# Optimization experiments

Measured on AMD Instinct MI355X. Metric: run time of the kernel, lower is better.

The kernel has to match this reference:

```python
import jax, jax.numpy as jnp
import numpy as np

N = 50000
E = 800000
D_IN = 64
D_HID = 64
N_CLASS = 40


def setup_inputs() -> dict:
    key = jax.random.key(0)
    ks = jax.random.split(key, 9)
    x = jax.random.normal(ks[0], (N, D_IN), dtype=jnp.float32)
    edge_index = jax.random.randint(ks[1], (2, E), 0, N, dtype=jnp.int64)
    # GCNConv weights (glorot-ish scale) and biases
    W1 = jax.random.normal(ks[2], (D_IN, D_HID), dtype=jnp.float32) / np.sqrt(D_IN)
    b1 = jnp.zeros((D_HID,), dtype=jnp.float32)
    W2 = jax.random.normal(ks[3], (D_HID, D_HID), dtype=jnp.float32) / np.sqrt(D_HID)
    b2 = jnp.zeros((D_HID,), dtype=jnp.float32)
    Wc = jax.random.normal(ks[4], (D_HID, N_CLASS), dtype=jnp.float32) / np.sqrt(D_HID)
    bc = jnp.zeros((N_CLASS,), dtype=jnp.float32)
    return {"x": x, "edge_index": edge_index, "W1": W1, "b1": b1,
            "W2": W2, "b2": b2, "Wc": Wc, "bc": bc}


def _gcn_conv(x, W, b, src, dst, n_nodes):
    """PyG GCNConv: add self-loops, sym-normalized mean aggregation, then +bias.
    out = D^{-1/2} (A + I) D^{-1/2} X W + b
    src/dst already include self-loops."""
    h = x @ W  # [N, D_out] -- transform before aggregation (fewer FLOPs if D_out<=D_in)
    deg = jax.ops.segment_sum(jnp.ones_like(dst, dtype=h.dtype), dst, num_segments=n_nodes)
    dinv = jnp.where(deg > 0, jax.lax.rsqrt(deg), 0.0)  # [N]
    norm = dinv[src] * dinv[dst]  # [E+N]
    msg = h[src] * norm[:, None]  # gather + scale
    out = jax.ops.segment_sum(msg, dst, num_segments=n_nodes)  # scatter-add
    return out + b


def reference(x, edge_index, W1, b1, W2, b2, Wc, bc):
    n = x.shape[0]
    loops = jnp.arange(n, dtype=edge_index.dtype)
    src = jnp.concatenate([edge_index[0], loops])
    dst = jnp.concatenate([edge_index[1], loops])
    h = jnp.tanh(_gcn_conv(x, W1, b1, src, dst, n))
    h = jnp.tanh(_gcn_conv(h, W2, b2, src, dst, n))
    out = h @ Wc + bc
    return (out, h)
```

## Files before the change

### kernel.cpp

```cpp
#include <hip/hip_runtime.h>
#include <math.h>

#define NN 50000
#define NE 800000
#define D 64
#define NC 40
#define NBUCK 196
#define SLAB 16384
#define EPB 4096

typedef unsigned short u16;
typedef unsigned int u32;

__device__ __forceinline__ u16 f32_to_bf16(float v) {
    u32 x = __float_as_uint(v);
    x += 0x7FFFu + ((x >> 16) & 1u);
    return (u16)(x >> 16);
}
__device__ __forceinline__ float bflo(u32 v) { return __uint_as_float(v << 16); }
__device__ __forceinline__ float bfhi(u32 v) { return __uint_as_float(v & 0xffff0000u); }


__global__ __launch_bounds__(256) void bucket_scatter(const int* __restrict__ ei,
                                                      int* __restrict__ cursor,
                                                      u32* __restrict__ slab) {
    __shared__ int sums[256];
    __shared__ int lofs[256];
    __shared__ int lcur[256];
    __shared__ int gbase[256];
    __shared__ int tot_s;
    __shared__ u32 sorted[EPB];
    __shared__ int gdest[EPB];
    int tid = threadIdx.x;

    u32 pk[16];
    int nmine = 0;
    int e0 = blockIdx.x * EPB + tid * 16;
    if (e0 < NE) {
        nmine = 16;
#pragma unroll
        for (int j = 0; j < 4; ++j) {
            int4 ss = *(const int4*)&ei[e0 + j * 4];
            int4 dd = *(const int4*)&ei[NE + e0 + j * 4];
            pk[j * 4 + 0] = ((u32)dd.x << 16) | (u32)ss.x;
            pk[j * 4 + 1] = ((u32)dd.y << 16) | (u32)ss.y;
            pk[j * 4 + 2] = ((u32)dd.z << 16) | (u32)ss.z;
            pk[j * 4 + 3] = ((u32)dd.w << 16) | (u32)ss.w;
        }
    }

    sums[tid] = 0;
    __syncthreads();
    for (int j = 0; j < nmine; ++j) atomicAdd(&sums[pk[j] >> 24], 1);
    __syncthreads();
    int v = sums[tid];
    __syncthreads();
    for (int off = 1; off < 256; off <<= 1) {
        int u = (tid >= off) ? sums[tid - off] : 0;
        __syncthreads();
        sums[tid] += u;
        __syncthreads();
    }
    lofs[tid] = sums[tid] - v;
    lcur[tid] = sums[tid] - v;
    if (tid == 255) tot_s = sums[255];
    if (tid < NBUCK) gbase[tid] = atomicAdd(&cursor[tid], v);
    __syncthreads();

    for (int j = 0; j < nmine; ++j) {
        u32 p = pk[j];
        int bin = (int)(p >> 24);
        int pos = atomicAdd(&lcur[bin], 1);
        sorted[pos] = p;
        gdest[pos] = bin * SLAB + gbase[bin] + (pos - lofs[bin]);
    }
    __syncthreads();

    int tot = tot_s;
    for (int i = tid; i < tot; i += 256) slab[gdest[i]] = sorted[i];
}


__global__ __launch_bounds__(256) void ell_build(const u32* __restrict__ slab,
                                                 const int* __restrict__ cursor,
                                                 u16* __restrict__ ell,
                                                 int* __restrict__ cnt,
                                                 float* __restrict__ dinv) {
    __shared__ u16 ell_lds[256 * 64];
    __shared__ int cnt_lds[256];
    int b = blockIdx.x, tid = threadIdx.x;
    uint4* z = (uint4*)ell_lds;
    for (int i = tid; i < 2048; i += 256) z[i] = make_uint4(0, 0, 0, 0);
    cnt_lds[tid] = 0;
    __syncthreads();

    int nE = cursor[b];
    const u32* run = slab + b * SLAB;
    int base = b * 256;
    for (int i = tid; i < nE; i += 256) {
        u32 p = run[i];
        int dl = (int)(p >> 16) - base;
        int r = atomicAdd(&cnt_lds[dl], 1);
        if (r < 64) ell_lds[dl * 64 + r] = (u16)(p & 0xffffu);
    }
    __syncthreads();

    int nNodes = NN - base; if (nNodes > 256) nNodes = 256;
    const uint4* s4 = (const uint4*)ell_lds;
    uint4* d4 = (uint4*)(ell + (size_t)base * 64);
    int n4 = nNodes * 8;
    for (int i = tid; i < n4; i += 256) d4[i] = s4[i];
    if (tid < nNodes) {
        int c = cnt_lds[tid];
        cnt[base + tid] = c;
        dinv[base + tid] = rsqrtf((float)c + 1.0f);
    }
}


__global__ __launch_bounds__(256) void gemm64_bf16(const float* __restrict__ A,
                                                   const float* __restrict__ W,
                                                   const float* __restrict__ dinv,
                                                   u16* __restrict__ C) {
    __shared__ float Ws[64 * 64];
    __shared__ float As[4 * 64];
    int tid = threadIdx.x;
    for (int i = tid; i < 64 * 64; i += 256) Ws[i] = W[i];
    int r = tid >> 6, c = tid & 63;
    int row = blockIdx.x * 4 + r;
    if (row < NN) As[r * 64 + c] = A[row * 64 + c];
    __syncthreads();
    if (row < NN) {
        float acc = 0.0f;
#pragma unroll
        for (int k = 0; k < 64; ++k) acc += As[r * 64 + k] * Ws[k * 64 + c];
        C[row * 64 + c] = f32_to_bf16(acc * dinv[row]);
    }
}


__device__ __forceinline__ void gather_pair_ell(const u16* __restrict__ ell,
                                                const int* __restrict__ cnt,
                                                const u32* __restrict__ hs32,
                                                int n0, int half, int p,
                                                u32* __restrict__ idxh,
                                                float& ox, float& oy) {
    int node = n0 + half;
    int deg0 = cnt[n0];     if (deg0 > 64) deg0 = 64;
    int deg1 = cnt[n0 + 1]; if (deg1 > 64) deg1 = 64;
    int deg = half ? deg1 : deg0;
    int degmax = (deg0 > deg1) ? deg0 : deg1;
    const u16* row = ell + node * 64;

    u32 sv = hs32[node * 32 + p];
    float ax = bflo(sv), ay = bfhi(sv);
    float bx = 0.0f, by = 0.0f;

    for (int base = 0; base < degmax; base += 32) {
        int slot = base + p;
        idxh[p] = (slot < deg) ? (u32)row[slot] : (u32)node;
        __builtin_amdgcn_wave_barrier();
        int n = degmax - base;
        if (n > 32) n = 32;
        for (int m0 = 0; m0 < n; m0 += 8) {
            u32 st[8];
#pragma unroll
            for (int u = 0; u < 8; ++u) {
                int src = (int)idxh[m0 + u];
                st[u] = hs32[src * 32 + p];
            }
#pragma unroll
            for (int u = 0; u < 8; ++u) {
                bool act = (base + m0 + u) < deg;
                float vx = act ? bflo(st[u]) : 0.0f;
                float vy = act ? bfhi(st[u]) : 0.0f;
                if (u & 1) { bx += vx; by += vy; } else { ax += vx; ay += vy; }
            }
        }
        __builtin_amdgcn_wave_barrier();
    }
    ox = ax + bx;
    oy = ay + by;
}


__global__ __launch_bounds__(256) void gather_l1_fused(const u16* __restrict__ ell,
                                                       const int* __restrict__ cnt,
                                                       const u16* __restrict__ hs,
                                                       const float* __restrict__ dinv,
                                                       const float* __restrict__ b1,
                                                       const float* __restrict__ W2,
                                                       u16* __restrict__ hs_out) {
    __shared__ float Ws[64 * 64];
    __shared__ __align__(16) float hb[4][2][64];
    __shared__ u32 idxb[4][2][32];
    int tid = threadIdx.x;
    for (int i = tid; i < 64 * 64; i += 256) Ws[i] = W2[i];
    __syncthreads();

    int r = tid >> 6, l = tid & 63, half = l >> 5, p = l & 31;
    int n0 = (blockIdx.x * 4 + r) * 2;
    int node = n0 + half;

    float gx, gy;
    gather_pair_ell(ell, cnt, (const u32*)hs, n0, half, p, idxb[r][half], gx, gy);

    float dv = dinv[node];
    float2 bb = *(const float2*)&b1[2 * p];
    float hx = tanhf(gx * dv + bb.x);
    float hy = tanhf(gy * dv + bb.y);
    *(float2*)&hb[r][half][2 * p] = make_float2(hx, hy);
    __builtin_amdgcn_wave_barrier();

    int d = l;
    float dv0 = dinv[n0], dv1 = dinv[n0 + 1];
    float acc0 = 0.0f, acc1 = 0.0f;
#pragma unroll
    for (int k4 = 0; k4 < 16; ++k4) {
        float4 h0 = *(const float4*)&hb[r][0][k4 * 4];
        float4 h1 = *(const float4*)&hb[r][1][k4 * 4];
        float w0 = Ws[(k4 * 4 + 0) * 64 + d];
        float w1 = Ws[(k4 * 4 + 1) * 64 + d];
        float w2 = Ws[(k4 * 4 + 2) * 64 + d];
        float w3 = Ws[(k4 * 4 + 3) * 64 + d];
        acc0 += h0.x * w0 + h0.y * w1 + h0.z * w2 + h0.w * w3;
        acc1 += h1.x * w0 + h1.y * w1 + h1.z * w2 + h1.w * w3;
    }
    hs_out[n0 * 64 + d] = f32_to_bf16(acc0 * dv0);
    hs_out[(n0 + 1) * 64 + d] = f32_to_bf16(acc1 * dv1);
}

__global__ __launch_bounds__(256) void gather_l2_fused(const u16* __restrict__ ell,
                                                       const int* __restrict__ cnt,
                                                       const u16* __restrict__ hs,
                                                       const float* __restrict__ dinv,
                                                       const float* __restrict__ b2,
                                                       const float* __restrict__ Wc,
                                                       const float* __restrict__ bc,
                                                       float* __restrict__ h_out,
                                                       float* __restrict__ out) {
    __shared__ float Ws[64 * NC];
    __shared__ float bs[NC];
    __shared__ __align__(16) float hb[4][2][64];
    __shared__ u32 idxb[4][2][32];
    int tid = threadIdx.x;
    for (int i = tid; i < 64 * NC; i += 256) Ws[i] = Wc[i];
    if (tid < NC) bs[tid] = bc[tid];
    __syncthreads();

    int r = tid >> 6, l = tid & 63, half = l >> 5, p = l & 31;
    int n0 = (blockIdx.x * 4 + r) * 2;
    int node = n0 + half;

    float gx, gy;
    gather_pair_ell(ell, cnt, (const u32*)hs, n0, half, p, idxb[r][half], gx, gy);

    float dv = dinv[node];
    float2 bb = *(const float2*)&b2[2 * p];
    float hx = tanhf(gx * dv + bb.x);
    float hy = tanhf(gy * dv + bb.y);
    *(float2*)&h_out[node * 64 + 2 * p] = make_float2(hx, hy);
    *(float2*)&hb[r][half][2 * p] = make_float2(hx, hy);
    __builtin_amdgcn_wave_barrier();

    int d = l;
    int dc = (d < NC) ? d : NC - 1;
    float acc0 = bs[dc], acc1 = bs[dc];
#pragma unroll
    for (int k4 = 0; k4 < 16; ++k4) {
        float4 v0 = *(const float4*)&hb[r][0][k4 * 4];
        float4 v1 = *(const float4*)&hb[r][1][k4 * 4];
        float w0 = Ws[(k4 * 4 + 0) * NC + dc];
        float w1 = Ws[(k4 * 4 + 1) * NC + dc];
        float w2 = Ws[(k4 * 4 + 2) * NC + dc];
        float w3 = Ws[(k4 * 4 + 3) * NC + dc];
        acc0 += v0.x * w0 + v0.y * w1 + v0.z * w2 + v0.w * w3;
        acc1 += v1.x * w0 + v1.y * w1 + v1.z * w2 + v1.w * w3;
    }
    if (d < NC) {
        out[n0 * NC + d] = acc0;
        out[(n0 + 1) * NC + d] = acc1;
    }
}


extern "C" void kernel_launch(void* const* d_in, const int* in_sizes, int n_in,
                              void* d_out, int out_size, void* d_ws, size_t ws_size,
                              hipStream_t stream) {
    const float* x  = (const float*)d_in[0];
    const int*   ei = (const int*)d_in[1];
    const float* W1 = (const float*)d_in[2];
    const float* b1 = (const float*)d_in[3];
    const float* W2 = (const float*)d_in[4];
    const float* b2 = (const float*)d_in[5];
    const float* Wc = (const float*)d_in[6];
    const float* bc = (const float*)d_in[7];

    float* out   = (float*)d_out;
    float* h_out = out + NN * NC;

    u32*   slab   = (u32*)d_ws;
    int*   cursor = (int*)(slab + NBUCK * SLAB);
    int*   cnt    = cursor + 256;
    float* dinv   = (float*)(cnt + NN);
    u16*   ell    = (u16*)(dinv + NN);
    u16*   hsA    = ell + (size_t)NN * 64;
    u16*   hsB    = hsA + NN * D;

    const int scatBlocks  = (NE + EPB - 1) / EPB;
    const int nodeBlocks4 = (NN + 3) / 4;
    const int nodeBlocks8 = NN / 8;

    hipMemsetAsync(cursor, 0, NBUCK * sizeof(int), stream);
    bucket_scatter<<<scatBlocks, 256, 0, stream>>>(ei, cursor, slab);
    ell_build<<<NBUCK, 256, 0, stream>>>(slab, cursor, ell, cnt, dinv);

    gemm64_bf16<<<nodeBlocks4, 256, 0, stream>>>(x, W1, dinv, hsA);
    gather_l1_fused<<<nodeBlocks8, 256, 0, stream>>>(ell, cnt, hsA, dinv, b1, W2, hsB);
    gather_l2_fused<<<nodeBlocks8, 256, 0, stream>>>(ell, cnt, hsB, dinv, b2, Wc, bc,
                                                     h_out, out);
}
```

Before: 186.8 us.

## Gather four nodes per wave with 8-byte loads and shuffle-broadcast indices

The ELL gather is restructured so each 64-lane wave handles four nodes, 16 lanes per node, each lane loading 4 bf16 features (uint2) per neighbor. The LDS index staging and wave barriers are replaced by one vector load of the ELL row per lane plus __shfl broadcasts of packed 16-bit indices, with 16 outstanding loads per iteration. The fused dense epilogues now compute four output rows per wave, reusing each weight load across more nodes. Waves now run to the maximum degree of four nodes instead of two, which adds more masked work per wave.

```diff
diff --git a/kernel.cpp b/kernel.cpp
--- a/kernel.cpp
+++ b/kernel.cpp
@@ -139,48 +139,48 @@
 }
 
 
-__device__ __forceinline__ void gather_pair_ell(const u16* __restrict__ ell,
-                                                const int* __restrict__ cnt,
-                                                const u32* __restrict__ hs32,
-                                                int n0, int half, int p,
-                                                u32* __restrict__ idxh,
-                                                float& ox, float& oy) {
-    int node = n0 + half;
-    int deg0 = cnt[n0];     if (deg0 > 64) deg0 = 64;
-    int deg1 = cnt[n0 + 1]; if (deg1 > 64) deg1 = 64;
-    int deg = half ? deg1 : deg0;
-    int degmax = (deg0 > deg1) ? deg0 : deg1;
-    const u16* row = ell + node * 64;
-
-    u32 sv = hs32[node * 32 + p];
-    float ax = bflo(sv), ay = bfhi(sv);
-    float bx = 0.0f, by = 0.0f;
-
-    for (int base = 0; base < degmax; base += 32) {
-        int slot = base + p;
-        idxh[p] = (slot < deg) ? (u32)row[slot] : (u32)node;
-        __builtin_amdgcn_wave_barrier();
-        int n = degmax - base;
-        if (n > 32) n = 32;
-        for (int m0 = 0; m0 < n; m0 += 8) {
-            u32 st[8];
-#pragma unroll
-            for (int u = 0; u < 8; ++u) {
-                int src = (int)idxh[m0 + u];
-                st[u] = hs32[src * 32 + p];
-            }
-#pragma unroll
-            for (int u = 0; u < 8; ++u) {
-                bool act = (base + m0 + u) < deg;
-                float vx = act ? bflo(st[u]) : 0.0f;
-                float vy = act ? bfhi(st[u]) : 0.0f;
-                if (u & 1) { bx += vx; by += vy; } else { ax += vx; ay += vy; }
-            }
+__device__ __forceinline__ void gather_quad(const u16* __restrict__ ell,
+                                            const int* __restrict__ cnt,
+                                            const uint2* __restrict__ hs2,
+                                            int base, int l,
+                                            float& a0, float& a1, float& a2, float& a3) {
+    int q = l >> 4, p = l & 15;
+    int node = base + q;
+    int4 c4 = *(const int4*)&cnt[base];
+    int d0 = c4.x > 64 ? 64 : c4.x;
+    int d1 = c4.y > 64 ? 64 : c4.y;
+    int d2 = c4.z > 64 ? 64 : c4.z;
+    int d3 = c4.w > 64 ? 64 : c4.w;
+    int deg = (q == 0) ? d0 : ((q == 1) ? d1 : ((q == 2) ? d2 : d3));
+    int m01 = (d0 > d1) ? d0 : d1;
+    int m23 = (d2 > d3) ? d2 : d3;
+    int degmax = (m01 > m23) ? m01 : m23;
+
+    uint2 iv = ((const uint2*)(ell + (size_t)node * 64))[p];
+
+    uint2 sv = hs2[node * 16 + p];
+    a0 = bflo(sv.x); a1 = bfhi(sv.x); a2 = bflo(sv.y); a3 = bfhi(sv.y);
+    float e0 = 0.0f, e1 = 0.0f, e2 = 0.0f, e3 = 0.0f;
+
+    for (int m = 0; m < degmax; m += 16) {
+        uint2 st[16];
+#pragma unroll
+        for (int u = 0; u < 16; ++u) {
+            u32 wsel = ((u >> 1) & 1) ? iv.y : iv.x;
+            int bc = __shfl((int)wsel, (l & 48) + (m >> 2) + (u >> 2));
+            int sid = (u & 1) ? (int)((u32)bc >> 16) : (int)(bc & 0xffff);
+            st[u] = hs2[sid * 16 + p];
         }
-        __builtin_amdgcn_wave_barrier();
-    }
-    ox = ax + bx;
-    oy = ay + by;
+#pragma unroll
+        for (int u = 0; u < 16; ++u) {
+            bool act = (m + u) < deg;
+            u32 x = act ? st[u].x : 0u;
+            u32 y = act ? st[u].y : 0u;
+            if (u & 1) { e0 += bflo(x); e1 += bfhi(x); e2 += bflo(y); e3 += bfhi(y); }
+            else       { a0 += bflo(x); a1 += bfhi(x); a2 += bflo(y); a3 += bfhi(y); }
+        }
+    }
+    a0 += e0; a1 += e1; a2 += e2; a3 += e3;
 }
 
 
@@ -192,42 +192,47 @@
                                                        const float* __restrict__ W2,
                                                        u16* __restrict__ hs_out) {
     __shared__ float Ws[64 * 64];
-    __shared__ __align__(16) float hb[4][2][64];
-    __shared__ u32 idxb[4][2][32];
+    __shared__ __align__(16) float hb[4][4][64];
     int tid = threadIdx.x;
     for (int i = tid; i < 64 * 64; i += 256) Ws[i] = W2[i];
     __syncthreads();
 
-    int r = tid >> 6, l = tid & 63, half = l >> 5, p = l & 31;
-    int n0 = (blockIdx.x * 4 + r) * 2;
-    int node = n0 + half;
-
-    float gx, gy;
-    gather_pair_ell(ell, cnt, (const u32*)hs, n0, half, p, idxb[r][half], gx, gy);
+    int r = tid >> 6, l = tid & 63, q = l >> 4, p = l & 15;
+    int base = (blockIdx.x * 4 + r) * 4;
+    int node = base + q;
+
+    float a0, a1, a2, a3;
+    gather_quad(ell, cnt, (const uint2*)hs, base, l, a0, a1, a2, a3);
 
     float dv = dinv[node];
-    float2 bb = *(const float2*)&b1[2 * p];
-    float hx = tanhf(gx * dv + bb.x);
-    float hy = tanhf(gy * dv + bb.y);
-    *(float2*)&hb[r][half][2 * p] = make_float2(hx, hy);
+    float4 bb = *(const float4*)&b1[p * 4];
+    float4 h = make_float4(tanhf(a0 * dv + bb.x), tanhf(a1 * dv + bb.y),
+                           tanhf(a2 * dv + bb.z), tanhf(a3 * dv + bb.w));
+    *(float4*)&hb[r][q][p * 4] = h;
     __builtin_amdgcn_wave_barrier();
 
     int d = l;
-    float dv0 = dinv[n0], dv1 = dinv[n0 + 1];
-    float acc0 = 0.0f, acc1 = 0.0f;
+    float4 dvv = *(const float4*)&dinv[base];
+    float o0 = 0.0f, o1 = 0.0f, o2 = 0.0f, o3 = 0.0f;
 #pragma unroll
     for (int k4 = 0; k4 < 16; ++k4) {
         float4 h0 = *(const float4*)&hb[r][0][k4 * 4];
         float4 h1 = *(const float4*)&hb[r][1][k4 * 4];
+        float4 h2 = *(const float4*)&hb[r][2][k4 * 4];
+        float4 h3 = *(const float4*)&hb[r][3][k4 * 4];
         float w0 = Ws[(k4 * 4 + 0) * 64 + d];
         float w1 = Ws[(k4 * 4 + 1) * 64 + d];
         float w2 = Ws[(k4 * 4 + 2) * 64 + d];
         float w3 = Ws[(k4 * 4 + 3) * 64 + d];
-        acc0 += h0.x * w0 + h0.y * w1 + h0.z * w2 + h0.w * w3;
-        acc1 += h1.x * w0 + h1.y * w1 + h1.z * w2 + h1.w * w3;
-    }
-    hs_out[n0 * 64 + d] = f32_to_bf16(acc0 * dv0);
-    hs_out[(n0 + 1) * 64 + d] = f32_to_bf16(acc1 * dv1);
+        o0 += h0.x * w0 + h0.y * w1 + h0.z * w2 + h0.w * w3;
+        o1 += h1.x * w0 + h1.y * w1 + h1.z * w2 + h1.w * w3;
+        o2 += h2.x * w0 + h2.y * w1 + h2.z * w2 + h2.w * w3;
+        o3 += h3.x * w0 + h3.y * w1 + h3.z * w2 + h3.w * w3;
+    }
+    hs_out[(base + 0) * 64 + d] = f32_to_bf16(o0 * dvv.x);
+    hs_out[(base + 1) * 64 + d] = f32_to_bf16(o1 * dvv.y);
+    hs_out[(base + 2) * 64 + d] = f32_to_bf16(o2 * dvv.z);
+    hs_out[(base + 3) * 64 + d] = f32_to_bf16(o3 * dvv.w);
 }
 
 __global__ __launch_bounds__(256) void gather_l2_fused(const u16* __restrict__ ell,
@@ -241,45 +246,51 @@
                                                        float* __restrict__ out) {
     __shared__ float Ws[64 * NC];
     __shared__ float bs[NC];
-    __shared__ __align__(16) float hb[4][2][64];
-    __shared__ u32 idxb[4][2][32];
+    __shared__ __align__(16) float hb[4][4][64];
     int tid = threadIdx.x;
     for (int i = tid; i < 64 * NC; i += 256) Ws[i] = Wc[i];
     if (tid < NC) bs[tid] = bc[tid];
     __syncthreads();
 
-    int r = tid >> 6, l = tid & 63, half = l >> 5, p = l & 31;
-    int n0 = (blockIdx.x * 4 + r) * 2;
-    int node = n0 + half;
-
-    float gx, gy;
-    gather_pair_ell(ell, cnt, (const u32*)hs, n0, half, p, idxb[r][half], gx, gy);
+    int r = tid >> 6, l = tid & 63, q = l >> 4, p = l & 15;
+    int base = (blockIdx.x * 4 + r) * 4;
+    int node = base + q;
+
+    float a0, a1, a2, a3;
+    gather_quad(ell, cnt, (const uint2*)hs, base, l, a0, a1, a2, a3);
 
     float dv = dinv[node];
-    float2 bb = *(const float2*)&b2[2 * p];
-    float hx = tanhf(gx * dv + bb.x);
-    float hy = tanhf(gy * dv + bb.y);
-    *(float2*)&h_out[node * 64 + 2 * p] = make_float2(hx, hy);
-    *(float2*)&hb[r][half][2 * p] = make_float2(hx, hy);
+    float4 bb = *(const float4*)&b2[p * 4];
+    float4 h = make_float4(tanhf(a0 * dv + bb.x), tanhf(a1 * dv + bb.y),
+                           tanhf(a2 * dv + bb.z), tanhf(a3 * dv + bb.w));
+    *(float4*)&h_out[node * 64 + p * 4] = h;
+    *(float4*)&hb[r][q][p * 4] = h;
     __builtin_amdgcn_wave_barrier();
 
     int d = l;
     int dc = (d < NC) ? d : NC - 1;
-    float acc0 = bs[dc], acc1 = bs[dc];
+    float bcd = bs[dc];
+    float o0 = bcd, o1 = bcd, o2 = bcd, o3 = bcd;
 #pragma unroll
     for (int k4 = 0; k4 < 16; ++k4) {
         float4 v0 = *(const float4*)&hb[r][0][k4 * 4];
         float4 v1 = *(const float4*)&hb[r][1][k4 * 4];
+        float4 v2 = *(const float4*)&hb[r][2][k4 * 4];
+        float4 v3 = *(const float4*)&hb[r][3][k4 * 4];
         float w0 = Ws[(k4 * 4 + 0) * NC + dc];
         float w1 = Ws[(k4 * 4 + 1) * NC + dc];
         float w2 = Ws[(k4 * 4 + 2) * NC + dc];
         float w3 = Ws[(k4 * 4 + 3) * NC + dc];
-        acc0 += v0.x * w0 + v0.y * w1 + v0.z * w2 + v0.w * w3;
-        acc1 += v1.x * w0 + v1.y * w1 + v1.z * w2 + v1.w * w3;
+        o0 += v0.x * w0 + v0.y * w1 + v0.z * w2 + v0.w * w3;
+        o1 += v1.x * w0 + v1.y * w1 + v1.z * w2 + v1.w * w3;
+        o2 += v2.x * w0 + v2.y * w1 + v2.z * w2 + v2.w * w3;
+        o3 += v3.x * w0 + v3.y * w1 + v3.z * w2 + v3.w * w3;
     }
     if (d < NC) {
-        out[n0 * NC + d] = acc0;
-        out[(n0 + 1) * NC + d] = acc1;
+        out[(base + 0) * NC + d] = o0;
+        out[(base + 1) * NC + d] = o1;
+        out[(base + 2) * NC + d] = o2;
+        out[(base + 3) * NC + d] = o3;
     }
 }
 
@@ -307,16 +318,16 @@
     u16*   hsA    = ell + (size_t)NN * 64;
     u16*   hsB    = hsA + NN * D;
 
-    const int scatBlocks  = (NE + EPB - 1) / EPB;
-    const int nodeBlocks4 = (NN + 3) / 4;
-    const int nodeBlocks8 = NN / 8;
+    const int scatBlocks   = (NE + EPB - 1) / EPB;
+    const int nodeBlocks4  = (NN + 3) / 4;
+    const int nodeBlocks16 = NN / 16;
 
     hipMemsetAsync(cursor, 0, NBUCK * sizeof(int), stream);
     bucket_scatter<<<scatBlocks, 256, 0, stream>>>(ei, cursor, slab);
     ell_build<<<NBUCK, 256, 0, stream>>>(slab, cursor, ell, cnt, dinv);
 
     gemm64_bf16<<<nodeBlocks4, 256, 0, stream>>>(x, W1, dinv, hsA);
-    gather_l1_fused<<<nodeBlocks8, 256, 0, stream>>>(ell, cnt, hsA, dinv, b1, W2, hsB);
-    gather_l2_fused<<<nodeBlocks8, 256, 0, stream>>>(ell, cnt, hsB, dinv, b2, Wc, bc,
-                                                     h_out, out);
-}
+    gather_l1_fused<<<nodeBlocks16, 256, 0, stream>>>(ell, cnt, hsA, dinv, b1, W2, hsB);
+    gather_l2_fused<<<nodeBlocks16, 256, 0, stream>>>(ell, cnt, hsB, dinv, b2, Wc, bc,
+                                                      h_out, out);
+}
```

Measured after the change: 181.1 us. 3.0% less time.
